# Performance work log

Hardware: AMD Instinct MI355X
Metric: run time of the kernel (lower is better)

## Reference

```python
import jax, jax.numpy as jnp
import numpy as np

THRESHOLD = 0.5
NEG_POS_RATIO = 3
ALPHA = 10.0
N_PRIORS = 8732
N_CLASSES = 21
BATCH = 128
N_OBJ = 32


def cxcy_to_xy(cxcy):
    return jnp.concatenate([cxcy[..., :2] - cxcy[..., 2:] / 2.0,
                            cxcy[..., :2] + cxcy[..., 2:] / 2.0], axis=-1)


def xy_to_cxcy(xy):
    return jnp.concatenate([(xy[..., :2] + xy[..., 2:]) / 2.0,
                            xy[..., 2:] - xy[..., :2]], axis=-1)


def cxcy_to_gcxgcy(cxcy, priors_cxcy):
    return jnp.concatenate([(cxcy[..., :2] - priors_cxcy[..., :2]) / (priors_cxcy[..., 2:] / 10.0),
                            jnp.log(cxcy[..., 2:] / priors_cxcy[..., 2:]) * 5.0], axis=-1)


def find_jaccard_overlap(a, b):
    # a: (M,4) xyxy, b: (P,4) xyxy -> (M,P)
    lt = jnp.maximum(a[:, None, :2], b[None, :, :2])
    rb = jnp.minimum(a[:, None, 2:], b[None, :, 2:])
    wh = jnp.clip(rb - lt, 0.0)
    inter = wh[..., 0] * wh[..., 1]
    area_a = (a[:, 2] - a[:, 0]) * (a[:, 3] - a[:, 1])
    area_b = (b[:, 2] - b[:, 0]) * (b[:, 3] - b[:, 1])
    return inter / (area_a[:, None] + area_b[None, :] - inter)


def _match_one(boxes, labels, priors_xy, priors_cxcy):
    # boxes: (M,4) xyxy, labels: (M,)
    iou = find_jaccard_overlap(boxes, priors_xy)           # (M,P)
    obj_idx = jnp.argmax(iou, axis=1)                      # best prior per object
    iou = iou.at[jnp.arange(boxes.shape[0]), obj_idx].set(1.0)
    positive = (iou >= THRESHOLD).any(axis=0)              # (P,)
    max_prior_idx = jnp.argmax(iou, axis=0)                # best object per prior
    true_cls = labels[max_prior_idx] * positive.astype(labels.dtype)
    matched = boxes[max_prior_idx]                         # (P,4)
    true_locs = cxcy_to_gcxgcy(xy_to_cxcy(matched), priors_cxcy)
    return true_locs, true_cls, positive


def setup_inputs() -> dict:
    key = jax.random.key(0)
    k1, k2, k3, k4, k5, k6 = jax.random.split(key, 6)
    pred_loc = jax.random.normal(k1, (BATCH, N_PRIORS, 4), dtype=jnp.float32)
    pred_cls = jax.random.normal(k2, (BATCH, N_PRIORS, N_CLASSES), dtype=jnp.float32)
    # valid xyxy gt boxes in [0,1]
    p1 = jax.random.uniform(k3, (BATCH, N_OBJ, 2))
    p2 = jax.random.uniform(k4, (BATCH, N_OBJ, 2))
    b_boxes = jnp.concatenate([jnp.minimum(p1, p2), jnp.maximum(p1, p2) + 1e-3], axis=-1)
    b_boxes = jnp.clip(b_boxes, 0.0, 1.0).astype(jnp.float32)
    b_labels = jax.random.randint(k5, (BATCH, N_OBJ), 1, N_CLASSES)
    cxy = jax.random.uniform(k6, (N_PRIORS, 2), minval=0.1, maxval=0.9)
    wh = jax.random.uniform(jax.random.fold_in(k6, 1), (N_PRIORS, 2), minval=0.05, maxval=0.3)
    priors_cxcy = jnp.concatenate([cxy, wh], axis=-1).astype(jnp.float32)
    return {"pred_loc": pred_loc, "pred_cls": pred_cls, "b_boxes": b_boxes,
            "b_labels": b_labels, "priors_cxcy": priors_cxcy}


def reference(pred_loc, pred_cls, b_boxes, b_labels, priors_cxcy):
    batch_size, n_priors, n_classes = pred_cls.shape
    priors_xy = cxcy_to_xy(priors_cxcy)
    true_locs, true_classes, positive = jax.vmap(
        _match_one, in_axes=(0, 0, None, None))(b_boxes, b_labels, priors_xy, priors_cxcy)
    pos_f = positive.astype(pred_loc.dtype)                 # (B,P)
    n_positives = positive.sum(axis=1)                      # (B,)
    n_pos_total = n_positives.sum().astype(pred_loc.dtype)
    # L1 loss (mean over positive box elements)
    loc_loss = (jnp.abs(pred_loc - true_locs) * pos_f[..., None]).sum() / (n_pos_total * 4.0)
    # per-prior cross-entropy
    logp = jax.nn.log_softmax(pred_cls, axis=-1)
    ce = -jnp.take_along_axis(logp, true_classes[..., None], axis=-1)[..., 0]  # (B,P)
    conf_loss_pos = (ce * pos_f).sum()
    # hard negative mining: sort negatives descending per image
    conf_neg = jnp.where(positive, 0.0, ce)
    conf_neg_sorted = -jnp.sort(-conf_neg, axis=1)
    ranks = jnp.arange(n_priors)[None, :]
    hard_mask = ranks < (NEG_POS_RATIO * n_positives)[:, None]
    conf_loss_hard_neg = jnp.where(hard_mask, conf_neg_sorted, 0.0).sum()
    conf_loss = (conf_loss_hard_neg + conf_loss_pos) / n_pos_total
    loc_loss = ALPHA * loc_loss
    total_loss = conf_loss + loc_loss
    return total_loss, loc_loss, conf_loss
```

## Files before the change

kernel.cpp:

```cpp
#include <hip/hip_runtime.h>
#include <math.h>

#define B 128
#define M 32
#define P 8732
#define C 21
#define ALPHA 10.0f
#define TPB2 256
#define PPT 4
#define PPB (TPB2 * PPT)
#define NB2 9

__global__ __launch_bounds__(256) void k1_objargmax(
    const float* __restrict__ b_boxes, const float* __restrict__ priors,
    int* __restrict__ objidx, int* __restrict__ done) {
  if (blockIdx.x == 0 && threadIdx.x == 0) *done = 0;
  int wid = threadIdx.x >> 6;
  int lane = threadIdx.x & 63;
  int b = blockIdx.x >> 1;
  int obase = ((blockIdx.x & 1) * 4 + wid) * 4;

  float ox1[4], oy1[4], ox2[4], oy2[4], oarea[4];
  float bI[4], bU[4];
  int bidx[4];
#pragma unroll
  for (int k = 0; k < 4; k++) {
    float4 bx = ((const float4*)b_boxes)[(size_t)b * M + obase + k];
    ox1[k] = bx.x; oy1[k] = bx.y; ox2[k] = bx.z; oy2[k] = bx.w;
    oarea[k] = (bx.z - bx.x) * (bx.w - bx.y);
    bI[k] = -1.0f; bU[k] = 1.0f; bidx[k] = P;
  }

#pragma unroll 4
  for (int p = lane; p < P; p += 64) {
    float4 pr = ((const float4*)priors)[p];
    float pw2 = pr.z * 0.5f, ph2 = pr.w * 0.5f;
    float px1 = pr.x - pw2, py1 = pr.y - ph2;
    float px2 = pr.x + pw2, py2 = pr.y + ph2;
    float areaP = pr.z * pr.w;
#pragma unroll
    for (int k = 0; k < 4; k++) {
      float iw = fminf(ox2[k], px2) - fmaxf(ox1[k], px1);
      float ih = fminf(oy2[k], py2) - fmaxf(oy1[k], py1);
      iw = fmaxf(iw, 0.0f);
      ih = fmaxf(ih, 0.0f);
      float inter = iw * ih;
      float uni = oarea[k] + areaP - inter;
      if (inter * bU[k] > bI[k] * uni) { bI[k] = inter; bU[k] = uni; bidx[k] = p; }
    }
  }
  for (int off = 32; off >= 1; off >>= 1) {
#pragma unroll
    for (int k = 0; k < 4; k++) {
      float oI = __shfl_xor(bI[k], off, 64);
      float oU = __shfl_xor(bU[k], off, 64);
      int oi = __shfl_xor(bidx[k], off, 64);
      float l = oI * bU[k], r = bI[k] * oU;
      if (l > r || (l == r && oi < bidx[k])) { bI[k] = oI; bU[k] = oU; bidx[k] = oi; }
    }
  }
  if (lane == 0) {
#pragma unroll
    for (int k = 0; k < 4; k++) objidx[(size_t)b * M + obase + k] = bidx[k];
  }
}

__global__ __launch_bounds__(TPB2) void k2_perprior(
    const float* __restrict__ pred_loc, const float* __restrict__ pred_cls,
    const float* __restrict__ b_boxes, const int* __restrict__ b_labels,
    const float* __restrict__ priors, const int* __restrict__ objidx,
    float* __restrict__ ploc, float* __restrict__ pce, int* __restrict__ pnp,
    float* __restrict__ confneg) {
  int b = blockIdx.y;
  int p0 = blockIdx.x * PPB;
  int tid = threadIdx.x;

  __shared__ float sx1[M], sy1[M], sx2[M], sy2[M], sarea[M];
  __shared__ int slab[M], sobj[M];
  if (tid < M) {
    int m = tid;
    float4 bx = ((const float4*)b_boxes)[b * M + m];
    sx1[m] = bx.x; sy1[m] = bx.y; sx2[m] = bx.z; sy2[m] = bx.w;
    sarea[m] = (bx.z - bx.x) * (bx.w - bx.y);
    slab[m] = b_labels[b * M + m];
    sobj[m] = objidx[b * M + m];
  }
  __syncthreads();

  float locpart = 0.0f, cepospart = 0.0f;
  int npos = 0;
  int pbase = p0 + tid * PPT;
  if (pbase < P) {
    float4 pr[PPT], pl[PPT];
    const float4* prp = (const float4*)priors + pbase;
    const float4* plp = (const float4*)pred_loc + (size_t)b * P + pbase;
#pragma unroll
    for (int j = 0; j < PPT; j++) { pr[j] = prp[j]; pl[j] = plp[j]; }

    float px1[PPT], py1[PPT], px2[PPT], py2[PPT], areaP[PPT];
    float bI[PPT], bU[PPT];
    int bm[PPT];
#pragma unroll
    for (int j = 0; j < PPT; j++) {
      float pw2 = pr[j].z * 0.5f, ph2 = pr[j].w * 0.5f;
      px1[j] = pr[j].x - pw2; py1[j] = pr[j].y - ph2;
      px2[j] = pr[j].x + pw2; py2[j] = pr[j].y + ph2;
      areaP[j] = pr[j].z * pr[j].w;
      bI[j] = -1.0f; bU[j] = 1.0f; bm[j] = 0;
    }
    for (int m = 0; m < M; m++) {
      float bx1 = sx1[m], by1 = sy1[m], bx2 = sx2[m], by2 = sy2[m];
      float ar = sarea[m];
      int so = sobj[m];
#pragma unroll
      for (int j = 0; j < PPT; j++) {
        float iw = fminf(bx2, px2[j]) - fmaxf(bx1, px1[j]);
        float ih = fminf(by2, py2[j]) - fmaxf(by1, py1[j]);
        iw = fmaxf(iw, 0.0f);
        ih = fmaxf(ih, 0.0f);
        float inter = iw * ih;
        float uni = ar + areaP[j] - inter;
        if (so == pbase + j) { inter = 1.0f; uni = 1.0f; }
        if (inter * bU[j] > bI[j] * uni) { bI[j] = inter; bU[j] = uni; bm[j] = m; }
      }
    }

    const float4* pc4t =
        (const float4*)(pred_cls + ((size_t)b * P + p0) * C) + 21 * tid;
    float4 cn;
    float* cnp = (float*)&cn;
#pragma unroll
    for (int j = 0; j < PPT; j++) {
      bool pos = (2.0f * bI[j] >= bU[j]);
      int mj = bm[j];
      int cls = pos ? slab[mj] : 0;
      float bx1 = sx1[mj], by1 = sy1[mj], bx2 = sx2[mj], by2 = sy2[mj];
      float cx = (bx1 + bx2) * 0.5f, cy = (by1 + by2) * 0.5f;
      float w = bx2 - bx1, h = by2 - by1;
      float g0 = (cx - pr[j].x) * 10.0f / pr[j].z;
      float g1 = (cy - pr[j].y) * 10.0f / pr[j].w;
      float g2 = __logf(w / pr[j].z) * 5.0f;
      float g3 = __logf(h / pr[j].w) * 5.0f;
      if (pos) {
        locpart += fabsf(pl[j].x - g0) + fabsf(pl[j].y - g1) +
                   fabsf(pl[j].z - g2) + fabsf(pl[j].w - g3);
        npos++;
      }
      float4 u4[6];
#pragma unroll
      for (int q = 0; q < 6; q++) u4[q] = pc4t[5 * j + q];
      const float* u = (const float*)u4;
      float mx = u[j];
#pragma unroll
      for (int c = 1; c < C; c++) mx = fmaxf(mx, u[j + c]);
      float se = 0.0f;
      float vc = u[j];
#pragma unroll
      for (int c = 0; c < C; c++) {
        float x = u[j + c];
        se += __expf(x - mx);
        if (c == cls) vc = x;
      }
      float ce = mx + __logf(se) - vc;
      cnp[j] = pos ? 0.0f : ce;
      cepospart += pos ? ce : 0.0f;
    }
    ((float4*)confneg)[((size_t)b * P + pbase) >> 2] = cn;
  }

  for (int off = 32; off >= 1; off >>= 1) {
    locpart += __shfl_down(locpart, off, 64);
    cepospart += __shfl_down(cepospart, off, 64);
    npos += __shfl_down(npos, off, 64);
  }
  __shared__ float rloc[4], rce[4];
  __shared__ int rnp[4];
  int wid = tid >> 6;
  if ((tid & 63) == 0) { rloc[wid] = locpart; rce[wid] = cepospart; rnp[wid] = npos; }
  __syncthreads();
  if (tid == 0) {
    int f = b * NB2 + blockIdx.x;
    ploc[f] = rloc[0] + rloc[1] + rloc[2] + rloc[3];
    pce[f] = rce[0] + rce[1] + rce[2] + rce[3];
    pnp[f] = rnp[0] + rnp[1] + rnp[2] + rnp[3];
  }
}

__global__ __launch_bounds__(1024) void k3_hardneg(
    const float* __restrict__ confneg,
    const float* __restrict__ ploc, const float* __restrict__ pce,
    const int* __restrict__ pnp,
    float* __restrict__ imgres, int* __restrict__ done,
    float* __restrict__ out) {
  int b = blockIdx.x;
  int tid = threadIdx.x;
  int wid = tid >> 6;
  int lane = tid & 63;

  __shared__ __align__(16) float s[P];
  __shared__ int histw[16 * 256];
  __shared__ __align__(16) int cnt[256];
  __shared__ int sdig, scum, sK, sLast;
  __shared__ float sLoc, sCe, sNp;
  __shared__ float rsum[16], rl[16], rc[16], rh[16], rn[16];
  __shared__ int rcnt[16];

  {
    const float4* row4 = (const float4*)(confneg + (size_t)b * P);
    for (int i = tid; i < P / 4; i += 1024) ((float4*)s)[i] = row4[i];
  }

  if (wid == 0) {
    float lp = 0.0f, cp = 0.0f;
    int np = 0;
    if (lane < NB2) {
      int f = b * NB2 + lane;
      lp = ploc[f]; cp = pce[f]; np = pnp[f];
    }
    for (int off = 32; off >= 1; off >>= 1) {
      lp += __shfl_down(lp, off, 64);
      cp += __shfl_down(cp, off, 64);
      np += __shfl_down(np, off, 64);
    }
    if (lane == 0) {
      int K = np * 3;
      if (K > P) K = P;
      sK = K; sLoc = lp; sCe = cp; sNp = (float)np;
    }
  }
  __syncthreads();

  int K = sK;
  unsigned pfx = 0;
  int Krem = K;
#pragma unroll
  for (int pass = 3; pass >= 0; --pass) {
    int sh = pass * 8;
    for (int i = tid; i < 16 * 256; i += 1024) histw[i] = 0;
    __syncthreads();
    unsigned himask = (pass == 3) ? 0u : (0xFFFFFFFFu << (sh + 8));
    int* myh = &histw[wid * 256];
    for (int i = tid; i < P; i += 1024) {
      unsigned ub = __float_as_uint(s[i]);
      if ((ub & himask) == pfx) atomicAdd(&myh[(ub >> sh) & 255], 1);
    }
    __syncthreads();
    if (tid < 256) {
      int c = 0;
#pragma unroll
      for (int w = 0; w < 16; w++) c += histw[w * 256 + tid];
      cnt[tid] = c;
    }
    __syncthreads();
    if (wid == 0) {
      int4 c4 = ((const int4*)cnt)[lane];
      int s3 = c4.w;
      int s2 = c4.z + s3;
      int s1 = c4.y + s2;
      int s0 = c4.x + s1;
      int suf = s0;
      for (int off = 1; off < 64; off <<= 1) {
        int t = __shfl_down(suf, off, 64);
        if (lane + off < 64) suf += t;
      }
      int above = suf - s0;
      int S0 = above + s0, S1 = above + s1, S2 = above + s2, S3 = above + s3;
      int S4 = above;
      if (S3 >= Krem && S4 < Krem) { sdig = 4 * lane + 3; scum = S4; }
      else if (S2 >= Krem && S3 < Krem) { sdig = 4 * lane + 2; scum = S3; }
      else if (S1 >= Krem && S2 < Krem) { sdig = 4 * lane + 1; scum = S2; }
      else if (S0 >= Krem && S1 < Krem) { sdig = 4 * lane + 0; scum = S1; }
    }
    __syncthreads();
    pfx |= ((unsigned)sdig) << sh;
    Krem -= scum;
  }
  float tau = __uint_as_float(pfx);

  float sum = 0.0f;
  int cgt = 0;
  for (int i = tid; i < P; i += 1024) {
    float v = s[i];
    if (v > tau) { sum += v; cgt++; }
  }
  for (int off = 32; off >= 1; off >>= 1) {
    sum += __shfl_down(sum, off, 64);
    cgt += __shfl_down(cgt, off, 64);
  }
  if (lane == 0) { rsum[wid] = sum; rcnt[wid] = cgt; }
  __syncthreads();
  if (tid == 0) {
    float stot = 0.0f;
    int ctot = 0;
#pragma unroll
    for (int w = 0; w < 16; w++) { stot += rsum[w]; ctot += rcnt[w]; }
    float hard = stot + (float)(K - ctot) * tau;
    imgres[b * 4 + 0] = sLoc;
    imgres[b * 4 + 1] = sCe;
    imgres[b * 4 + 2] = hard;
    imgres[b * 4 + 3] = sNp;
    __threadfence();
    int prev = atomicAdd(done, 1);
    sLast = (prev == B - 1) ? 1 : 0;
  }
  __syncthreads();
  if (sLast) {
    __threadfence();
    float l = 0.0f, c = 0.0f, h = 0.0f, n = 0.0f;
    if (tid < B) {
      l = atomicAdd(&imgres[tid * 4 + 0], 0.0f);
      c = atomicAdd(&imgres[tid * 4 + 1], 0.0f);
      h = atomicAdd(&imgres[tid * 4 + 2], 0.0f);
      n = atomicAdd(&imgres[tid * 4 + 3], 0.0f);
    }
    for (int off = 32; off >= 1; off >>= 1) {
      l += __shfl_down(l, off, 64);
      c += __shfl_down(c, off, 64);
      h += __shfl_down(h, off, 64);
      n += __shfl_down(n, off, 64);
    }
    if (lane == 0) { rl[wid] = l; rc[wid] = c; rh[wid] = h; rn[wid] = n; }
    __syncthreads();
    if (tid == 0) {
      float L = 0, Cc = 0, H = 0, N = 0;
#pragma unroll
      for (int w = 0; w < 16; w++) { L += rl[w]; Cc += rc[w]; H += rh[w]; N += rn[w]; }
      float loc = ALPHA * L / (N * 4.0f);
      float conf = (H + Cc) / N;
      out[0] = conf + loc;
      out[1] = loc;
      out[2] = conf;
    }
  }
}

extern "C" void kernel_launch(void* const* d_in, const int* in_sizes, int n_in,
                              void* d_out, int out_size, void* d_ws, size_t ws_size,
                              hipStream_t stream) {
  (void)in_sizes; (void)n_in; (void)out_size; (void)ws_size;
  const float* pred_loc = (const float*)d_in[0];
  const float* pred_cls = (const float*)d_in[1];
  const float* b_boxes = (const float*)d_in[2];
  const int* b_labels = (const int*)d_in[3];
  const float* priors = (const float*)d_in[4];
  float* out = (float*)d_out;

  int* done = (int*)d_ws;
  float* ploc = (float*)d_ws + 8;
  float* pce = ploc + B * NB2;
  int* pnp = (int*)(pce + B * NB2);
  float* imgres = (float*)(pnp + B * NB2);
  int* objidx = (int*)(imgres + B * 4);
  float* confneg = (float*)(objidx + B * M);

  k1_objargmax<<<B * 2, 256, 0, stream>>>(b_boxes, priors, objidx, done);
  dim3 g2(NB2, B);
  k2_perprior<<<g2, TPB2, 0, stream>>>(pred_loc, pred_cls, b_boxes, b_labels,
                                       priors, objidx, ploc, pce, pnp, confneg);
  k3_hardneg<<<B, 1024, 0, stream>>>(confneg, ploc, pce, pnp, imgres, done, out);
}
```

Baseline: 239.0 us.

## Split object-argmax over prior chunks and skip loc work for negative-only waves

The per-object best-prior search is split across 8 prior chunks per image, so there are 1024 blocks instead of 256, and a new small kernel reduces the partial argmax results. In the per-prior kernel, the pred_loc loads and box encoding run only when some lane in the wave has a positive prior, and the positive-class CE extraction is likewise gated by that wave-level vote. Divisions are replaced with hardware reciprocals. This adds a kernel launch and workspace traffic, and the reduction tie-breaking across chunks relies on strict comparison order.

```diff
diff --git a/kernel.cpp b/kernel.cpp
--- a/kernel.cpp
+++ b/kernel.cpp
@@ -10,36 +10,41 @@
 #define PPT 4
 #define PPB (TPB2 * PPT)
 #define NB2 9
-
-__global__ __launch_bounds__(256) void k1_objargmax(
+#define CH 8
+#define CS 1092
+
+__global__ __launch_bounds__(256) void k1_partial(
     const float* __restrict__ b_boxes, const float* __restrict__ priors,
-    int* __restrict__ objidx, int* __restrict__ done) {
+    float* __restrict__ pI, float* __restrict__ pU, int* __restrict__ pidx,
+    int* __restrict__ done) {
   if (blockIdx.x == 0 && threadIdx.x == 0) *done = 0;
+  int b = blockIdx.x >> 3;
+  int ch = blockIdx.x & 7;
   int wid = threadIdx.x >> 6;
   int lane = threadIdx.x & 63;
-  int b = blockIdx.x >> 1;
-  int obase = ((blockIdx.x & 1) * 4 + wid) * 4;
-
-  float ox1[4], oy1[4], ox2[4], oy2[4], oarea[4];
-  float bI[4], bU[4];
-  int bidx[4];
-#pragma unroll
-  for (int k = 0; k < 4; k++) {
+  int obase = wid * 8;
+
+  float ox1[8], oy1[8], ox2[8], oy2[8], oarea[8], bI[8], bU[8];
+  int bidx[8];
+#pragma unroll
+  for (int k = 0; k < 8; k++) {
     float4 bx = ((const float4*)b_boxes)[(size_t)b * M + obase + k];
     ox1[k] = bx.x; oy1[k] = bx.y; ox2[k] = bx.z; oy2[k] = bx.w;
     oarea[k] = (bx.z - bx.x) * (bx.w - bx.y);
     bI[k] = -1.0f; bU[k] = 1.0f; bidx[k] = P;
   }
 
-#pragma unroll 4
-  for (int p = lane; p < P; p += 64) {
+  int pend = (ch + 1) * CS;
+  if (pend > P) pend = P;
+#pragma unroll 2
+  for (int p = ch * CS + lane; p < pend; p += 64) {
     float4 pr = ((const float4*)priors)[p];
     float pw2 = pr.z * 0.5f, ph2 = pr.w * 0.5f;
     float px1 = pr.x - pw2, py1 = pr.y - ph2;
     float px2 = pr.x + pw2, py2 = pr.y + ph2;
     float areaP = pr.z * pr.w;
 #pragma unroll
-    for (int k = 0; k < 4; k++) {
+    for (int k = 0; k < 8; k++) {
       float iw = fminf(ox2[k], px2) - fmaxf(ox1[k], px1);
       float ih = fminf(oy2[k], py2) - fmaxf(oy1[k], py1);
       iw = fmaxf(iw, 0.0f);
@@ -51,7 +56,7 @@
   }
   for (int off = 32; off >= 1; off >>= 1) {
 #pragma unroll
-    for (int k = 0; k < 4; k++) {
+    for (int k = 0; k < 8; k++) {
       float oI = __shfl_xor(bI[k], off, 64);
       float oU = __shfl_xor(bU[k], off, 64);
       int oi = __shfl_xor(bidx[k], off, 64);
@@ -61,8 +66,27 @@
   }
   if (lane == 0) {
 #pragma unroll
-    for (int k = 0; k < 4; k++) objidx[(size_t)b * M + obase + k] = bidx[k];
-  }
+    for (int k = 0; k < 8; k++) {
+      int idx = ((size_t)b * M + obase + k) * CH + ch;
+      pI[idx] = bI[k]; pU[idx] = bU[k]; pidx[idx] = bidx[k];
+    }
+  }
+}
+
+__global__ __launch_bounds__(256) void k1_reduce(
+    const float* __restrict__ pI, const float* __restrict__ pU,
+    const int* __restrict__ pidx, int* __restrict__ objidx) {
+  int o = blockIdx.x * 256 + threadIdx.x;
+  if (o >= B * M) return;
+  float cI = pI[o * CH], cU = pU[o * CH];
+  int ci = pidx[o * CH];
+#pragma unroll
+  for (int ch = 1; ch < CH; ch++) {
+    float nI = pI[o * CH + ch], nU = pU[o * CH + ch];
+    int ni = pidx[o * CH + ch];
+    if (nI * cU > cI * nU) { cI = nI; cU = nU; ci = ni; }
+  }
+  objidx[o] = ci;
 }
 
 __global__ __launch_bounds__(TPB2) void k2_perprior(
@@ -91,11 +115,10 @@
   int npos = 0;
   int pbase = p0 + tid * PPT;
   if (pbase < P) {
-    float4 pr[PPT], pl[PPT];
+    float4 pr[PPT];
     const float4* prp = (const float4*)priors + pbase;
-    const float4* plp = (const float4*)pred_loc + (size_t)b * P + pbase;
-#pragma unroll
-    for (int j = 0; j < PPT; j++) { pr[j] = prp[j]; pl[j] = plp[j]; }
+#pragma unroll
+    for (int j = 0; j < PPT; j++) pr[j] = prp[j];
 
     float px1[PPT], py1[PPT], px2[PPT], py2[PPT], areaP[PPT];
     float bI[PPT], bU[PPT];
@@ -125,27 +148,40 @@
       }
     }
 
+    bool pos[PPT];
+#pragma unroll
+    for (int j = 0; j < PPT; j++) pos[j] = (2.0f * bI[j] >= bU[j]);
+    int wAny = __any((int)(pos[0] | pos[1] | pos[2] | pos[3]));
+
+    if (wAny) {
+      const float4* plp = (const float4*)pred_loc + (size_t)b * P + pbase;
+#pragma unroll
+      for (int j = 0; j < PPT; j++) {
+        float4 pl = plp[j];
+        int mj = bm[j];
+        float bx1 = sx1[mj], by1 = sy1[mj], bx2 = sx2[mj], by2 = sy2[mj];
+        float cx = (bx1 + bx2) * 0.5f, cy = (by1 + by2) * 0.5f;
+        float w = bx2 - bx1, h = by2 - by1;
+        float rz = __builtin_amdgcn_rcpf(pr[j].z);
+        float rw = __builtin_amdgcn_rcpf(pr[j].w);
+        float g0 = (cx - pr[j].x) * 10.0f * rz;
+        float g1 = (cy - pr[j].y) * 10.0f * rw;
+        float g2 = __logf(w * rz) * 5.0f;
+        float g3 = __logf(h * rw) * 5.0f;
+        if (pos[j]) {
+          locpart += fabsf(pl.x - g0) + fabsf(pl.y - g1) +
+                     fabsf(pl.z - g2) + fabsf(pl.w - g3);
+          npos++;
+        }
+      }
+    }
+
     const float4* pc4t =
         (const float4*)(pred_cls + ((size_t)b * P + p0) * C) + 21 * tid;
     float4 cn;
     float* cnp = (float*)&cn;
 #pragma unroll
     for (int j = 0; j < PPT; j++) {
-      bool pos = (2.0f * bI[j] >= bU[j]);
-      int mj = bm[j];
-      int cls = pos ? slab[mj] : 0;
-      float bx1 = sx1[mj], by1 = sy1[mj], bx2 = sx2[mj], by2 = sy2[mj];
-      float cx = (bx1 + bx2) * 0.5f, cy = (by1 + by2) * 0.5f;
-      float w = bx2 - bx1, h = by2 - by1;
-      float g0 = (cx - pr[j].x) * 10.0f / pr[j].z;
-      float g1 = (cy - pr[j].y) * 10.0f / pr[j].w;
-      float g2 = __logf(w / pr[j].z) * 5.0f;
-      float g3 = __logf(h / pr[j].w) * 5.0f;
-      if (pos) {
-        locpart += fabsf(pl[j].x - g0) + fabsf(pl[j].y - g1) +
-                   fabsf(pl[j].z - g2) + fabsf(pl[j].w - g3);
-        npos++;
-      }
       float4 u4[6];
 #pragma unroll
       for (int q = 0; q < 6; q++) u4[q] = pc4t[5 * j + q];
@@ -154,16 +190,18 @@
 #pragma unroll
       for (int c = 1; c < C; c++) mx = fmaxf(mx, u[j + c]);
       float se = 0.0f;
-      float vc = u[j];
-#pragma unroll
-      for (int c = 0; c < C; c++) {
-        float x = u[j + c];
-        se += __expf(x - mx);
-        if (c == cls) vc = x;
+#pragma unroll
+      for (int c = 0; c < C; c++) se += __expf(u[j + c] - mx);
+      float lse = mx + __logf(se);
+      cnp[j] = pos[j] ? 0.0f : (lse - u[j]);
+      if (wAny) {
+        int cls = pos[j] ? slab[bm[j]] : 0;
+        float vc = u[j];
+#pragma unroll
+        for (int c = 1; c < C; c++)
+          if (c == cls) vc = u[j + c];
+        cepospart += pos[j] ? (lse - vc) : 0.0f;
       }
-      float ce = mx + __logf(se) - vc;
-      cnp[j] = pos ? 0.0f : ce;
-      cepospart += pos ? ce : 0.0f;
     }
     ((float4*)confneg)[((size_t)b * P + pbase) >> 2] = cn;
   }
@@ -350,10 +388,14 @@
   float* pce = ploc + B * NB2;
   int* pnp = (int*)(pce + B * NB2);
   float* imgres = (float*)(pnp + B * NB2);
-  int* objidx = (int*)(imgres + B * 4);
+  float* pI = imgres + B * 4;
+  float* pU = pI + B * M * CH;
+  int* pidx = (int*)(pU + B * M * CH);
+  int* objidx = pidx + B * M * CH;
   float* confneg = (float*)(objidx + B * M);
 
-  k1_objargmax<<<B * 2, 256, 0, stream>>>(b_boxes, priors, objidx, done);
+  k1_partial<<<B * CH, 256, 0, stream>>>(b_boxes, priors, pI, pU, pidx, done);
+  k1_reduce<<<(B * M + 255) / 256, 256, 0, stream>>>(pI, pU, pidx, objidx);
   dim3 g2(NB2, B);
   k2_perprior<<<g2, TPB2, 0, stream>>>(pred_loc, pred_cls, b_boxes, b_labels,
                                        priors, objidx, ploc, pce, pnp, confneg);
```

After: 225.4 us. 5.7% less time.
